# Optimization experiments

Hardware: AMD Instinct MI355X
Metric: run time of the kernel (lower is better)

## Reference

```python
import jax, jax.numpy as jnp
import numpy as np

BS, N, F, R, OUT = 8, 512, 512, 16, 512
ALPHA = 0.2

def setup_inputs() -> dict:
    key = jax.random.key(0)
    ks = jax.random.split(key, 16)
    w = lambda k, shp: (jax.random.normal(k, shp, dtype=jnp.float32) * 0.05)
    return {
        'x_ori': jax.random.normal(ks[0], (BS, N, F), dtype=jnp.float32),
        'x': jax.random.normal(ks[1], (BS, N, F), dtype=jnp.float32),
        'c': jax.random.normal(ks[2], (BS, 1, F), dtype=jnp.float32),
        'adj': jax.random.randint(ks[3], (BS, N, N, R), 0, 2, dtype=jnp.int32),
        'Wfc': w(ks[4], (F, F)),
        'Wdc': w(ks[5], (F, F)),
        'Wqv': w(ks[6], (2 * F, F)),
        'Wkv': w(ks[7], (2 * F, F)),
        'Wqc': w(ks[8], (F, F)),
        'Wkc': w(ks[9], (F, F)),
        'Wa': w(ks[10], (2 * F, R)),
        'Wu': w(ks[11], (2 * F, OUT)),
    }

def reference(x_ori, x, c, adj, Wfc, Wdc, Wqv, Wkv, Wqc, Wkc, Wa, Wu):
    # relation-context modulation vector m: [bs,1,F]
    m = jnp.matmul(jax.nn.elu(jnp.matmul(c, Wfc)), Wdc)
    nodes = jnp.concatenate([x, x_ori], axis=2)          # [bs,N,2F]
    xq = jnp.matmul(nodes, Wqv) * jnp.matmul(m, Wqc)     # [bs,N,F]
    xk = jnp.matmul(nodes, Wkv) * jnp.matmul(m, Wkc)     # [bs,N,F]
    # scores[b,i,j,r] = leakyrelu(xq_i . Wa[:F,r] + xk_j . Wa[F:,r])
    # (equivalent to cat([xq_i,xk_j]) @ Wa without materializing [bs,N,N,2F])
    sq = jnp.matmul(xq, Wa[:F])                          # [bs,N,R]
    sk = jnp.matmul(xk, Wa[F:])                          # [bs,N,R]
    scores = jax.nn.leaky_relu(sq[:, :, None, :] + sk[:, None, :, :], ALPHA)
    adj_f = adj.astype(scores.dtype)                     # [bs,N,N,R]
    s = jnp.sum(scores * adj_f, axis=3)                  # [bs,N,N]
    mask = jnp.sum(adj_f, axis=3) > 0
    attn = jax.nn.softmax(jnp.where(mask, s, jnp.float32(-9e15)), axis=2)
    new_x = jnp.matmul(attn, x)                          # [bs,N,F]
    return jnp.matmul(jnp.concatenate([x, new_x], axis=2), Wu)
```

## Files before the change

kernel.cpp:

```cpp
#include <hip/hip_runtime.h>
#include <hip/hip_bf16.h>
#include <cstddef>
#include <cstdint>

static constexpr int BSZ  = 8;
static constexpr int NN   = 512;
static constexpr int FF   = 512;
static constexpr int RR   = 16;
static constexpr int TWOF = 1024;

typedef __attribute__((ext_vector_type(8))) short short8;
typedef __attribute__((ext_vector_type(4))) float f32x4;

__device__ __forceinline__ ushort bf16_bits(float v) {
    union { __hip_bfloat16 h; ushort u; } cvt;
    cvt.h = __float2bfloat16(v);
    return cvt.u;
}

static constexpr size_t OFF_TB     = 0;
static constexpr size_t OFF_MB     = 16384;
static constexpr size_t OFF_MQ     = 32768;
static constexpr size_t OFF_MK     = 49152;
static constexpr size_t OFF_SQ     = 65536;
static constexpr size_t OFF_SK     = 327680;
static constexpr size_t OFF_WQET   = 589824;
static constexpr size_t OFF_WKET   = 851968;
static constexpr size_t OFF_ATTN   = 1114112;
static constexpr size_t OFF_XBF    = 5308416;
static constexpr size_t OFF_XTBF   = 9502720;
static constexpr size_t OFF_XORIBF = 13697024;
static constexpr size_t OFF_NEWXBF = 17891328;
static constexpr size_t OFF_WUT    = 22085632;

__global__ __launch_bounds__(256) void k_prep(
    const float* __restrict__ x_ori, const float* __restrict__ x,
    const float* __restrict__ Wu,
    ushort* __restrict__ xori_bf, ushort* __restrict__ x_bf,
    ushort* __restrict__ xT_bf, ushort* __restrict__ WuT)
{
    int blk = blockIdx.x;
    int t = threadIdx.x;
    if (blk < 1024) {
        int idx = blk * 256 + t;
        float4 a = ((const float4*)x_ori)[idx * 2];
        float4 b = ((const float4*)x_ori)[idx * 2 + 1];
        uint4 s;
        s.x = (uint)bf16_bits(a.x) | ((uint)bf16_bits(a.y) << 16);
        s.y = (uint)bf16_bits(a.z) | ((uint)bf16_bits(a.w) << 16);
        s.z = (uint)bf16_bits(b.x) | ((uint)bf16_bits(b.y) << 16);
        s.w = (uint)bf16_bits(b.z) | ((uint)bf16_bits(b.w) << 16);
        ((uint4*)xori_bf)[idx] = s;
    } else if (blk < 3072) {
        __shared__ float tile[32][33];
        int bb = blk - 1024;
        int f0 = (bb & 15) * 32, i0 = ((bb >> 4) & 15) * 32, b = bb >> 8;
        int cc = t & 31, r0 = t >> 5;
#pragma unroll
        for (int rr = 0; rr < 32; rr += 8) {
            int i = i0 + r0 + rr;
            float v = x[((size_t)b * NN + i) * FF + f0 + cc];
            tile[r0 + rr][cc] = v;
            x_bf[((size_t)b * NN + i) * FF + f0 + cc] = bf16_bits(v);
        }
        __syncthreads();
#pragma unroll
        for (int rr = 0; rr < 32; rr += 8) {
            int f = f0 + r0 + rr;
            xT_bf[((size_t)b * FF + f) * NN + i0 + cc] = bf16_bits(tile[cc][r0 + rr]);
        }
    } else {
        __shared__ float tile2[32][33];
        int bb = blk - 3072;
        int f0 = (bb & 31) * 32, o0 = (bb >> 5) * 32;
        int cc = t & 31, r0 = t >> 5;
#pragma unroll
        for (int rr = 0; rr < 32; rr += 8)
            tile2[r0 + rr][cc] = Wu[(size_t)(f0 + r0 + rr) * FF + o0 + cc];
        __syncthreads();
#pragma unroll
        for (int rr = 0; rr < 32; rr += 8)
            WuT[(size_t)(o0 + r0 + rr) * TWOF + f0 + cc] = bf16_bits(tile2[cc][r0 + rr]);
    }
}

__global__ __launch_bounds__(256) void k_matvec(const float* __restrict__ vin,
                                                const float* __restrict__ W,
                                                float* __restrict__ vout,
                                                int elu_out) {
    __shared__ float red[8][32];
    int b = blockIdx.y;
    int f0 = blockIdx.x * 32;
    int t = threadIdx.x;
    int f = t & 31, kq = t >> 5;
    const float* vb = vin + (size_t)b * FF;
    float acc = 0.f;
    int ks = kq * 64;
#pragma unroll 8
    for (int k = ks; k < ks + 64; ++k)
        acc = fmaf(vb[k], W[(size_t)k * FF + f0 + f], acc);
    red[kq][f] = acc;
    __syncthreads();
    if (kq == 0) {
        acc += red[1][f] + red[2][f] + red[3][f] + red[4][f] +
               red[5][f] + red[6][f] + red[7][f];
        if (elu_out) acc = (acc > 0.f) ? acc : expm1f(acc);
        vout[(size_t)b * FF + f0 + f] = acc;
    }
}

__global__ __launch_bounds__(256) void k_mqk(const float* __restrict__ m,
                                             const float* __restrict__ Wqc,
                                             const float* __restrict__ Wkc,
                                             float* __restrict__ mq,
                                             float* __restrict__ mk) {
    __shared__ float redq[8][32];
    __shared__ float redk[8][32];
    int b = blockIdx.y;
    int f0 = blockIdx.x * 32;
    int t = threadIdx.x;
    int f = t & 31, kq = t >> 5;
    const float* mb = m + (size_t)b * FF;
    float aq = 0.f, ak = 0.f;
    int ks = kq * 64;
#pragma unroll 8
    for (int k = ks; k < ks + 64; ++k) {
        float mv = mb[k];
        aq = fmaf(mv, Wqc[(size_t)k * FF + f0 + f], aq);
        ak = fmaf(mv, Wkc[(size_t)k * FF + f0 + f], ak);
    }
    redq[kq][f] = aq;
    redk[kq][f] = ak;
    __syncthreads();
    if (kq == 0) {
        aq += redq[1][f] + redq[2][f] + redq[3][f] + redq[4][f] +
              redq[5][f] + redq[6][f] + redq[7][f];
        ak += redk[1][f] + redk[2][f] + redk[3][f] + redk[4][f] +
              redk[5][f] + redk[6][f] + redk[7][f];
        mq[(size_t)b * FF + f0 + f] = aq;
        mk[(size_t)b * FF + f0 + f] = ak;
    }
}

__global__ __launch_bounds__(256) void k_weff(const float* __restrict__ Wqv,
                                              const float* __restrict__ Wkv,
                                              const float* __restrict__ Wa,
                                              const float* __restrict__ mqv,
                                              const float* __restrict__ mkv,
                                              ushort* __restrict__ WqEt,
                                              ushort* __restrict__ WkEt) {
    int z = blockIdx.z;
    const float* W = z ? Wkv : Wqv;
    const float* mvec = z ? mkv : mqv;
    ushort* WeffT = z ? WkEt : WqEt;
    int waRowOff = z ? FF : 0;

    __shared__ float4 wa4[FF * 4];
    int tid = threadIdx.x;
    int b = blockIdx.y;
    const float* mv = mvec + (size_t)b * FF;
#pragma unroll
    for (int qq = 0; qq < 8; ++qq) {
        int idx = tid + qq * 256;
        int f = idx >> 2, rq = idx & 3;
        float4 w = *reinterpret_cast<const float4*>(Wa + (size_t)(waRowOff + f) * RR + rq * 4);
        float s = mv[f];
        float4 o;
        o.x = w.x * s; o.y = w.y * s; o.z = w.z * s; o.w = w.w * s;
        wa4[idx] = o;
    }
    __syncthreads();
    int k_l = tid >> 2, r4 = tid & 3;
    int k = blockIdx.x * 64 + k_l;
    const float4* Wrow4 = reinterpret_cast<const float4*>(W + (size_t)k * FF);
    float4 acc = {0.f, 0.f, 0.f, 0.f};
#pragma unroll 4
    for (int f4 = 0; f4 < FF / 4; ++f4) {
        float4 w = Wrow4[f4];
        float4 v0 = wa4[(f4 * 4 + 0) * 4 + r4];
        float4 v1 = wa4[(f4 * 4 + 1) * 4 + r4];
        float4 v2 = wa4[(f4 * 4 + 2) * 4 + r4];
        float4 v3 = wa4[(f4 * 4 + 3) * 4 + r4];
        acc.x = fmaf(w.x, v0.x, acc.x); acc.y = fmaf(w.x, v0.y, acc.y);
        acc.z = fmaf(w.x, v0.z, acc.z); acc.w = fmaf(w.x, v0.w, acc.w);
        acc.x = fmaf(w.y, v1.x, acc.x); acc.y = fmaf(w.y, v1.y, acc.y);
        acc.z = fmaf(w.y, v1.z, acc.z); acc.w = fmaf(w.y, v1.w, acc.w);
        acc.x = fmaf(w.z, v2.x, acc.x); acc.y = fmaf(w.z, v2.y, acc.y);
        acc.z = fmaf(w.z, v2.z, acc.z); acc.w = fmaf(w.z, v2.w, acc.w);
        acc.x = fmaf(w.w, v3.x, acc.x); acc.y = fmaf(w.w, v3.y, acc.y);
        acc.z = fmaf(w.w, v3.z, acc.z); acc.w = fmaf(w.w, v3.w, acc.w);
    }
    WeffT[((size_t)b * RR + r4 * 4 + 0) * TWOF + k] = bf16_bits(acc.x);
    WeffT[((size_t)b * RR + r4 * 4 + 1) * TWOF + k] = bf16_bits(acc.y);
    WeffT[((size_t)b * RR + r4 * 4 + 2) * TWOF + k] = bf16_bits(acc.z);
    WeffT[((size_t)b * RR + r4 * 4 + 3) * TWOF + k] = bf16_bits(acc.w);
}

__global__ __launch_bounds__(256) void k_sqsk(const ushort* __restrict__ x_bf,
                                              const ushort* __restrict__ xori_bf,
                                              const ushort* __restrict__ WqEt,
                                              const ushort* __restrict__ WkEt,
                                              float* __restrict__ sq,
                                              float* __restrict__ sk) {
    int t = threadIdx.x;
    int b = blockIdx.y;
    int m0 = blockIdx.x * 32;
    int lane = t & 63, w = t >> 6;
    int sub = w & 1, isK = w >> 1;
    int m_l = lane & 15, q = lane >> 4;
    int row = m0 + sub * 16 + m_l;
    const ushort* Bt = (isK ? WkEt : WqEt) + ((size_t)b * RR + m_l) * TWOF;
    f32x4 acc = {0.f, 0.f, 0.f, 0.f};
#pragma unroll
    for (int k0 = 0; k0 < TWOF; k0 += 32) {
        const ushort* src = (k0 < FF) ? x_bf : xori_bf;
        int kc = k0 & (FF - 1);
        short8 af = *(const short8*)(src + ((size_t)b * NN + row) * FF + kc + q * 8);
        short8 bf = *(const short8*)(Bt + k0 + q * 8);
        acc = __builtin_amdgcn_mfma_f32_16x16x32_bf16(af, bf, acc, 0, 0, 0);
    }
    float* dst = isK ? sk : sq;
#pragma unroll
    for (int r = 0; r < 4; ++r) {
        int i = m0 + sub * 16 + q * 4 + r;
        dst[((size_t)b * NN + i) * RR + m_l] = acc[r];
    }
}

__global__ __launch_bounds__(256) void k_attn(const int* __restrict__ adj,
                                              const float* __restrict__ sq,
                                              const float* __restrict__ sk,
                                              ushort* __restrict__ attn_bf) {
    int t = threadIdx.x;
    int i = blockIdx.x;
    int b = blockIdx.y;
    __shared__ float sqv_s[RR];
    __shared__ float redmax[4];
    __shared__ float redsum[4];
    __shared__ float bc_max;
    __shared__ float bc_sum;
    if (t < RR) sqv_s[t] = sq[((size_t)b * NN + i) * RR + t];
    __syncthreads();
    float sv[RR];
#pragma unroll
    for (int r = 0; r < RR; ++r) sv[r] = sqv_s[r];

    float z[2];
#pragma unroll
    for (int jj = 0; jj < 2; ++jj) {
        int j = t + jj * 256;
        size_t base = ((size_t)(b * NN + i) * NN + j) * RR;
        const int4* ap = reinterpret_cast<const int4*>(adj + base);
        int4 a0 = ap[0], a1 = ap[1], a2 = ap[2], a3 = ap[3];
        const float4* kp = reinterpret_cast<const float4*>(sk + ((size_t)b * NN + j) * RR);
        float4 s0 = kp[0], s1 = kp[1], s2 = kp[2], s3 = kp[3];
        int sum_adj = a0.x + a0.y + a0.z + a0.w + a1.x + a1.y + a1.z + a1.w +
                      a2.x + a2.y + a2.z + a2.w + a3.x + a3.y + a3.z + a3.w;
        float ssum = 0.f;
#define LR_TERM(SVAL, AVAL, RIDX)                                   \
        { float v_ = sv[RIDX] + (SVAL);                             \
          v_ = fmaxf(v_, 0.2f * v_);                                \
          ssum = fmaf(v_, (float)(AVAL), ssum); }
        LR_TERM(s0.x, a0.x, 0)  LR_TERM(s0.y, a0.y, 1)
        LR_TERM(s0.z, a0.z, 2)  LR_TERM(s0.w, a0.w, 3)
        LR_TERM(s1.x, a1.x, 4)  LR_TERM(s1.y, a1.y, 5)
        LR_TERM(s1.z, a1.z, 6)  LR_TERM(s1.w, a1.w, 7)
        LR_TERM(s2.x, a2.x, 8)  LR_TERM(s2.y, a2.y, 9)
        LR_TERM(s2.z, a2.z, 10) LR_TERM(s2.w, a2.w, 11)
        LR_TERM(s3.x, a3.x, 12) LR_TERM(s3.y, a3.y, 13)
        LR_TERM(s3.z, a3.z, 14) LR_TERM(s3.w, a3.w, 15)
#undef LR_TERM
        z[jj] = (sum_adj > 0) ? ssum : -9e15f;
    }

    int wv = t >> 6, ln = t & 63;
    float lm = fmaxf(z[0], z[1]);
    for (int off = 32; off; off >>= 1) lm = fmaxf(lm, __shfl_xor(lm, off, 64));
    if (ln == 0) redmax[wv] = lm;
    __syncthreads();
    if (t == 0) bc_max = fmaxf(fmaxf(redmax[0], redmax[1]), fmaxf(redmax[2], redmax[3]));
    __syncthreads();
    float mx = bc_max;
    float e0 = __expf(z[0] - mx);
    float e1 = __expf(z[1] - mx);
    float ls = e0 + e1;
    for (int off = 32; off; off >>= 1) ls += __shfl_xor(ls, off, 64);
    if (ln == 0) redsum[wv] = ls;
    __syncthreads();
    if (t == 0) bc_sum = redsum[0] + redsum[1] + redsum[2] + redsum[3];
    __syncthreads();
    float inv = 1.f / bc_sum;
    ushort* outp = attn_bf + (size_t)(b * NN + i) * NN;
    outp[t] = bf16_bits(e0 * inv);
    outp[t + 256] = bf16_bits(e1 * inv);
}

__global__ __launch_bounds__(256) void k_gemm(const ushort* __restrict__ A1, size_t sA1,
                                              const ushort* __restrict__ A2, size_t sA2,
                                              const ushort* __restrict__ BT, size_t sBT,
                                              float* __restrict__ Cf,
                                              ushort* __restrict__ Cb, size_t sC,
                                              int K, int ldBT) {
    __shared__ ushort As[2][64 * 40];
    __shared__ ushort Bs[2][64 * 40];
    int t = threadIdx.x;
    int n0 = blockIdx.x * 64, m0 = blockIdx.y * 64, b = blockIdx.z;
    int row = t >> 2, c8 = (t & 3) * 8;
    int lane = t & 63, w = t >> 6;
    int m_l = lane & 15, q = lane >> 4;
    f32x4 acc[4] = {{0.f,0.f,0.f,0.f},{0.f,0.f,0.f,0.f},{0.f,0.f,0.f,0.f},{0.f,0.f,0.f,0.f}};
    const ushort* BTb = BT + (size_t)b * sBT;
    for (int k0 = 0; k0 < K; k0 += 64) {
#pragma unroll
        for (int h = 0; h < 2; ++h) {
            int kk = k0 + h * 32;
            const ushort* Aab; int kc;
            if (kk < FF) { Aab = A1 + (size_t)b * sA1; kc = kk; }
            else         { Aab = A2 + (size_t)b * sA2; kc = kk - FF; }
            uint4 av = *(const uint4*)(Aab + (size_t)(m0 + row) * FF + kc + c8);
            uint4 bv = *(const uint4*)(BTb + (size_t)(n0 + row) * ldBT + kk + c8);
            *(uint4*)(&As[h][row * 40 + c8]) = av;
            *(uint4*)(&Bs[h][row * 40 + c8]) = bv;
        }
        __syncthreads();
#pragma unroll
        for (int h = 0; h < 2; ++h) {
            short8 af = *(const short8*)(&As[h][(w * 16 + m_l) * 40 + q * 8]);
#pragma unroll
            for (int nb = 0; nb < 4; ++nb) {
                short8 bfr = *(const short8*)(&Bs[h][(nb * 16 + m_l) * 40 + q * 8]);
                acc[nb] = __builtin_amdgcn_mfma_f32_16x16x32_bf16(af, bfr, acc[nb], 0, 0, 0);
            }
        }
        __syncthreads();
    }
#pragma unroll
    for (int nb = 0; nb < 4; ++nb) {
#pragma unroll
        for (int r = 0; r < 4; ++r) {
            int mi = m0 + w * 16 + q * 4 + r;
            int ni = n0 + nb * 16 + m_l;
            float v = acc[nb][r];
            if (Cb) Cb[(size_t)b * sC + (size_t)mi * FF + ni] = bf16_bits(v);
            else    Cf[(size_t)b * sC + (size_t)mi * FF + ni] = v;
        }
    }
}

extern "C" void kernel_launch(void* const* d_in, const int* in_sizes, int n_in,
                              void* d_out, int out_size, void* d_ws, size_t ws_size,
                              hipStream_t stream) {
    const float* x_ori = (const float*)d_in[0];
    const float* x     = (const float*)d_in[1];
    const float* c     = (const float*)d_in[2];
    const int*   adj   = (const int*)d_in[3];
    const float* Wfc   = (const float*)d_in[4];
    const float* Wdc   = (const float*)d_in[5];
    const float* Wqv   = (const float*)d_in[6];
    const float* Wkv   = (const float*)d_in[7];
    const float* Wqc   = (const float*)d_in[8];
    const float* Wkc   = (const float*)d_in[9];
    const float* Wa    = (const float*)d_in[10];
    const float* Wu    = (const float*)d_in[11];
    float* out = (float*)d_out;

    char* ws = (char*)d_ws;
    float*  tb      = (float*)(ws + OFF_TB);
    float*  mb      = (float*)(ws + OFF_MB);
    float*  mq      = (float*)(ws + OFF_MQ);
    float*  mk      = (float*)(ws + OFF_MK);
    float*  sq      = (float*)(ws + OFF_SQ);
    float*  sk      = (float*)(ws + OFF_SK);
    ushort* WqEt    = (ushort*)(ws + OFF_WQET);
    ushort* WkEt    = (ushort*)(ws + OFF_WKET);
    ushort* attn_bf = (ushort*)(ws + OFF_ATTN);
    ushort* x_bf    = (ushort*)(ws + OFF_XBF);
    ushort* xT_bf   = (ushort*)(ws + OFF_XTBF);
    ushort* xori_bf = (ushort*)(ws + OFF_XORIBF);
    ushort* newx_bf = (ushort*)(ws + OFF_NEWXBF);
    ushort* WuT     = (ushort*)(ws + OFF_WUT);

    dim3 blk(256);

    k_prep<<<dim3(3584), blk, 0, stream>>>(x_ori, x, Wu, xori_bf, x_bf, xT_bf, WuT);

    k_matvec<<<dim3(16, BSZ), blk, 0, stream>>>(c, Wfc, tb, 1);
    k_matvec<<<dim3(16, BSZ), blk, 0, stream>>>(tb, Wdc, mb, 0);
    k_mqk<<<dim3(16, BSZ), blk, 0, stream>>>(mb, Wqc, Wkc, mq, mk);

    k_weff<<<dim3(16, BSZ, 2), blk, 0, stream>>>(Wqv, Wkv, Wa, mq, mk, WqEt, WkEt);

    k_sqsk<<<dim3(16, BSZ), blk, 0, stream>>>(x_bf, xori_bf, WqEt, WkEt, sq, sk);

    k_attn<<<dim3(NN, BSZ), blk, 0, stream>>>(adj, sq, sk, attn_bf);

    k_gemm<<<dim3(8, 8, BSZ), blk, 0, stream>>>(
        attn_bf, (size_t)NN * NN, attn_bf, (size_t)NN * NN,
        xT_bf, (size_t)FF * NN, nullptr, newx_bf, (size_t)NN * FF, FF, NN);

    k_gemm<<<dim3(8, 8, BSZ), blk, 0, stream>>>(
        x_bf, (size_t)NN * FF, newx_bf, (size_t)NN * FF,
        WuT, (size_t)0, out, nullptr, (size_t)NN * FF, TWOF, TWOF);
}
```

Baseline: 308.2 us.

## Fuse masked softmax with attention-times-x GEMM and fold first matvec into prep

Replaces the per-row softmax kernel and the separate attn@x GEMM with one kernel. Each block computes masked scores for 16 query rows, keeps the softmax numerators in LDS as bf16, and multiplies them by x^T with MFMA, applying the 1/rowsum scale at the end. This removes the materialized bf16 attention matrix, its global round trip and one launch. The first c@Wfc+ELU matvec also moves into the prep kernel as extra blocks, dropping another launch. In exchange the grid shrinks from 4096 blocks to 256, which lowers parallelism for streaming the large adj tensor. The PV stage also reads x^T straight from global memory with no LDS tiling.

```diff
diff --git a/kernel.cpp b/kernel.cpp
--- a/kernel.cpp
+++ b/kernel.cpp
@@ -26,7 +26,6 @@
 static constexpr size_t OFF_SK     = 327680;
 static constexpr size_t OFF_WQET   = 589824;
 static constexpr size_t OFF_WKET   = 851968;
-static constexpr size_t OFF_ATTN   = 1114112;
 static constexpr size_t OFF_XBF    = 5308416;
 static constexpr size_t OFF_XTBF   = 9502720;
 static constexpr size_t OFF_XORIBF = 13697024;
@@ -35,9 +34,11 @@
 
 __global__ __launch_bounds__(256) void k_prep(
     const float* __restrict__ x_ori, const float* __restrict__ x,
+    const float* __restrict__ c, const float* __restrict__ Wfc,
     const float* __restrict__ Wu,
     ushort* __restrict__ xori_bf, ushort* __restrict__ x_bf,
-    ushort* __restrict__ xT_bf, ushort* __restrict__ WuT)
+    ushort* __restrict__ xT_bf, ushort* __restrict__ WuT,
+    float* __restrict__ tb)
 {
     int blk = blockIdx.x;
     int t = threadIdx.x;
@@ -69,7 +70,7 @@
             int f = f0 + r0 + rr;
             xT_bf[((size_t)b * FF + f) * NN + i0 + cc] = bf16_bits(tile[cc][r0 + rr]);
         }
-    } else {
+    } else if (blk < 3584) {
         __shared__ float tile2[32][33];
         int bb = blk - 3072;
         int f0 = (bb & 31) * 32, o0 = (bb >> 5) * 32;
@@ -81,13 +82,30 @@
 #pragma unroll
         for (int rr = 0; rr < 32; rr += 8)
             WuT[(size_t)(o0 + r0 + rr) * TWOF + f0 + cc] = bf16_bits(tile2[cc][r0 + rr]);
+    } else {
+        __shared__ float red1[8][32];
+        int bb = blk - 3584;
+        int b = bb >> 4, f0 = (bb & 15) * 32;
+        int f = t & 31, kq = t >> 5;
+        const float* vb = c + (size_t)b * FF;
+        float acc = 0.f;
+        int ks = kq * 64;
+#pragma unroll 8
+        for (int k = ks; k < ks + 64; ++k)
+            acc = fmaf(vb[k], Wfc[(size_t)k * FF + f0 + f], acc);
+        red1[kq][f] = acc;
+        __syncthreads();
+        if (kq == 0) {
+            acc += red1[1][f] + red1[2][f] + red1[3][f] + red1[4][f] +
+                   red1[5][f] + red1[6][f] + red1[7][f];
+            tb[(size_t)b * FF + f0 + f] = (acc > 0.f) ? acc : expm1f(acc);
+        }
     }
 }
 
 __global__ __launch_bounds__(256) void k_matvec(const float* __restrict__ vin,
                                                 const float* __restrict__ W,
-                                                float* __restrict__ vout,
-                                                int elu_out) {
+                                                float* __restrict__ vout) {
     __shared__ float red[8][32];
     int b = blockIdx.y;
     int f0 = blockIdx.x * 32;
@@ -104,7 +122,6 @@
     if (kq == 0) {
         acc += red[1][f] + red[2][f] + red[3][f] + red[4][f] +
                red[5][f] + red[6][f] + red[7][f];
-        if (elu_out) acc = (acc > 0.f) ? acc : expm1f(acc);
         vout[(size_t)b * FF + f0 + f] = acc;
     }
 }
@@ -227,79 +244,113 @@
     }
 }
 
-__global__ __launch_bounds__(256) void k_attn(const int* __restrict__ adj,
-                                              const float* __restrict__ sq,
-                                              const float* __restrict__ sk,
-                                              ushort* __restrict__ attn_bf) {
-    int t = threadIdx.x;
-    int i = blockIdx.x;
+__global__ __launch_bounds__(256) void k_attn_pv(const int* __restrict__ adj,
+                                                 const float* __restrict__ sq,
+                                                 const float* __restrict__ sk,
+                                                 const ushort* __restrict__ xT_bf,
+                                                 ushort* __restrict__ newx_bf) {
+    constexpr int ZS = 520;
+    __shared__ float  zbuf[16 * ZS];
+    __shared__ ushort P[16 * ZS];
+    __shared__ float  rowsum[16];
+    int t = threadIdx.x;
     int b = blockIdx.y;
-    __shared__ float sqv_s[RR];
-    __shared__ float redmax[4];
-    __shared__ float redsum[4];
-    __shared__ float bc_max;
-    __shared__ float bc_sum;
-    if (t < RR) sqv_s[t] = sq[((size_t)b * NN + i) * RR + t];
+    int m0 = blockIdx.x * 16;
+
+    {
+        int r = t >> 4, cc = t & 15;
+        int i = m0 + r;
+        const float4* sqp = (const float4*)(sq + ((size_t)b * NN + i) * RR);
+        float4 q0 = sqp[0], q1 = sqp[1], q2 = sqp[2], q3 = sqp[3];
+        float sv[16] = {q0.x, q0.y, q0.z, q0.w, q1.x, q1.y, q1.z, q1.w,
+                        q2.x, q2.y, q2.z, q2.w, q3.x, q3.y, q3.z, q3.w};
+#pragma unroll 4
+        for (int it = 0; it < 32; ++it) {
+            int j = it * 16 + cc;
+            size_t base = (((size_t)b * NN + i) * NN + j) * RR;
+            const int4* ap = (const int4*)(adj + base);
+            int4 a0 = ap[0], a1 = ap[1], a2 = ap[2], a3 = ap[3];
+            const float4* kp = (const float4*)(sk + ((size_t)b * NN + j) * RR);
+            float4 s0 = kp[0], s1 = kp[1], s2 = kp[2], s3 = kp[3];
+            int sum_adj = a0.x + a0.y + a0.z + a0.w + a1.x + a1.y + a1.z + a1.w +
+                          a2.x + a2.y + a2.z + a2.w + a3.x + a3.y + a3.z + a3.w;
+            float ssum = 0.f;
+#define LR_TERM(SVAL, AVAL, RIDX)                                   \
+            { float v_ = sv[RIDX] + (SVAL);                         \
+              v_ = fmaxf(v_, 0.2f * v_);                            \
+              ssum = fmaf(v_, (float)(AVAL), ssum); }
+            LR_TERM(s0.x, a0.x, 0)  LR_TERM(s0.y, a0.y, 1)
+            LR_TERM(s0.z, a0.z, 2)  LR_TERM(s0.w, a0.w, 3)
+            LR_TERM(s1.x, a1.x, 4)  LR_TERM(s1.y, a1.y, 5)
+            LR_TERM(s1.z, a1.z, 6)  LR_TERM(s1.w, a1.w, 7)
+            LR_TERM(s2.x, a2.x, 8)  LR_TERM(s2.y, a2.y, 9)
+            LR_TERM(s2.z, a2.z, 10) LR_TERM(s2.w, a2.w, 11)
+            LR_TERM(s3.x, a3.x, 12) LR_TERM(s3.y, a3.y, 13)
+            LR_TERM(s3.z, a3.z, 14) LR_TERM(s3.w, a3.w, 15)
+#undef LR_TERM
+            zbuf[r * ZS + j] = (sum_adj > 0) ? ssum : -9e15f;
+        }
+    }
     __syncthreads();
-    float sv[RR];
-#pragma unroll
-    for (int r = 0; r < RR; ++r) sv[r] = sqv_s[r];
-
-    float z[2];
-#pragma unroll
-    for (int jj = 0; jj < 2; ++jj) {
-        int j = t + jj * 256;
-        size_t base = ((size_t)(b * NN + i) * NN + j) * RR;
-        const int4* ap = reinterpret_cast<const int4*>(adj + base);
-        int4 a0 = ap[0], a1 = ap[1], a2 = ap[2], a3 = ap[3];
-        const float4* kp = reinterpret_cast<const float4*>(sk + ((size_t)b * NN + j) * RR);
-        float4 s0 = kp[0], s1 = kp[1], s2 = kp[2], s3 = kp[3];
-        int sum_adj = a0.x + a0.y + a0.z + a0.w + a1.x + a1.y + a1.z + a1.w +
-                      a2.x + a2.y + a2.z + a2.w + a3.x + a3.y + a3.z + a3.w;
-        float ssum = 0.f;
-#define LR_TERM(SVAL, AVAL, RIDX)                                   \
-        { float v_ = sv[RIDX] + (SVAL);                             \
-          v_ = fmaxf(v_, 0.2f * v_);                                \
-          ssum = fmaf(v_, (float)(AVAL), ssum); }
-        LR_TERM(s0.x, a0.x, 0)  LR_TERM(s0.y, a0.y, 1)
-        LR_TERM(s0.z, a0.z, 2)  LR_TERM(s0.w, a0.w, 3)
-        LR_TERM(s1.x, a1.x, 4)  LR_TERM(s1.y, a1.y, 5)
-        LR_TERM(s1.z, a1.z, 6)  LR_TERM(s1.w, a1.w, 7)
-        LR_TERM(s2.x, a2.x, 8)  LR_TERM(s2.y, a2.y, 9)
-        LR_TERM(s2.z, a2.z, 10) LR_TERM(s2.w, a2.w, 11)
-        LR_TERM(s3.x, a3.x, 12) LR_TERM(s3.y, a3.y, 13)
-        LR_TERM(s3.z, a3.z, 14) LR_TERM(s3.w, a3.w, 15)
-#undef LR_TERM
-        z[jj] = (sum_adj > 0) ? ssum : -9e15f;
-    }
-
-    int wv = t >> 6, ln = t & 63;
-    float lm = fmaxf(z[0], z[1]);
-    for (int off = 32; off; off >>= 1) lm = fmaxf(lm, __shfl_xor(lm, off, 64));
-    if (ln == 0) redmax[wv] = lm;
+
+    {
+        int w = t >> 6, lane = t & 63;
+        int rr = w * 4 + (lane >> 4);
+        int cc = lane & 15;
+        const float* zr = &zbuf[rr * ZS];
+        float mx = -3.0e38f;
+#pragma unroll 8
+        for (int it = 0; it < 32; ++it) mx = fmaxf(mx, zr[it * 16 + cc]);
+#pragma unroll
+        for (int off = 1; off < 16; off <<= 1) mx = fmaxf(mx, __shfl_xor(mx, off, 64));
+        float sum = 0.f;
+        ushort* pr = &P[rr * ZS];
+#pragma unroll 8
+        for (int it = 0; it < 32; ++it) {
+            float e = __expf(zr[it * 16 + cc] - mx);
+            pr[it * 16 + cc] = bf16_bits(e);
+            sum += e;
+        }
+#pragma unroll
+        for (int off = 1; off < 16; off <<= 1) sum += __shfl_xor(sum, off, 64);
+        if (cc == 0) rowsum[rr] = sum;
+    }
     __syncthreads();
-    if (t == 0) bc_max = fmaxf(fmaxf(redmax[0], redmax[1]), fmaxf(redmax[2], redmax[3]));
-    __syncthreads();
-    float mx = bc_max;
-    float e0 = __expf(z[0] - mx);
-    float e1 = __expf(z[1] - mx);
-    float ls = e0 + e1;
-    for (int off = 32; off; off >>= 1) ls += __shfl_xor(ls, off, 64);
-    if (ln == 0) redsum[wv] = ls;
-    __syncthreads();
-    if (t == 0) bc_sum = redsum[0] + redsum[1] + redsum[2] + redsum[3];
-    __syncthreads();
-    float inv = 1.f / bc_sum;
-    ushort* outp = attn_bf + (size_t)(b * NN + i) * NN;
-    outp[t] = bf16_bits(e0 * inv);
-    outp[t + 256] = bf16_bits(e1 * inv);
+
+    {
+        int w = t >> 6, lane = t & 63;
+        int m_l = lane & 15, q = lane >> 4;
+        int n0w = w * 128;
+        f32x4 acc[8] = {};
+        const ushort* xTb = xT_bf + (size_t)b * FF * NN;
+        for (int k0 = 0; k0 < NN; k0 += 32) {
+            short8 af = *(const short8*)(&P[m_l * ZS + k0 + q * 8]);
+#pragma unroll
+            for (int nb = 0; nb < 8; ++nb) {
+                int n = n0w + nb * 16 + m_l;
+                short8 bfr = *(const short8*)(xTb + (size_t)n * NN + k0 + q * 8);
+                acc[nb] = __builtin_amdgcn_mfma_f32_16x16x32_bf16(af, bfr, acc[nb], 0, 0, 0);
+            }
+        }
+        float inv[4];
+#pragma unroll
+        for (int rg = 0; rg < 4; ++rg) inv[rg] = 1.f / rowsum[q * 4 + rg];
+#pragma unroll
+        for (int nb = 0; nb < 8; ++nb) {
+#pragma unroll
+            for (int rg = 0; rg < 4; ++rg) {
+                int i = m0 + q * 4 + rg;
+                int f = n0w + nb * 16 + m_l;
+                newx_bf[((size_t)b * NN + i) * FF + f] = bf16_bits(acc[nb][rg] * inv[rg]);
+            }
+        }
+    }
 }
 
 __global__ __launch_bounds__(256) void k_gemm(const ushort* __restrict__ A1, size_t sA1,
                                               const ushort* __restrict__ A2, size_t sA2,
                                               const ushort* __restrict__ BT, size_t sBT,
-                                              float* __restrict__ Cf,
-                                              ushort* __restrict__ Cb, size_t sC,
+                                              float* __restrict__ Cf, size_t sC,
                                               int K, int ldBT) {
     __shared__ ushort As[2][64 * 40];
     __shared__ ushort Bs[2][64 * 40];
@@ -340,9 +391,7 @@
         for (int r = 0; r < 4; ++r) {
             int mi = m0 + w * 16 + q * 4 + r;
             int ni = n0 + nb * 16 + m_l;
-            float v = acc[nb][r];
-            if (Cb) Cb[(size_t)b * sC + (size_t)mi * FF + ni] = bf16_bits(v);
-            else    Cf[(size_t)b * sC + (size_t)mi * FF + ni] = v;
+            Cf[(size_t)b * sC + (size_t)mi * FF + ni] = acc[nb][r];
         }
     }
 }
@@ -373,7 +422,6 @@
     float*  sk      = (float*)(ws + OFF_SK);
     ushort* WqEt    = (ushort*)(ws + OFF_WQET);
     ushort* WkEt    = (ushort*)(ws + OFF_WKET);
-    ushort* attn_bf = (ushort*)(ws + OFF_ATTN);
     ushort* x_bf    = (ushort*)(ws + OFF_XBF);
     ushort* xT_bf   = (ushort*)(ws + OFF_XTBF);
     ushort* xori_bf = (ushort*)(ws + OFF_XORIBF);
@@ -382,23 +430,19 @@
 
     dim3 blk(256);
 
-    k_prep<<<dim3(3584), blk, 0, stream>>>(x_ori, x, Wu, xori_bf, x_bf, xT_bf, WuT);
-
-    k_matvec<<<dim3(16, BSZ), blk, 0, stream>>>(c, Wfc, tb, 1);
-    k_matvec<<<dim3(16, BSZ), blk, 0, stream>>>(tb, Wdc, mb, 0);
+    k_prep<<<dim3(3712), blk, 0, stream>>>(x_ori, x, c, Wfc, Wu,
+                                           xori_bf, x_bf, xT_bf, WuT, tb);
+
+    k_matvec<<<dim3(16, BSZ), blk, 0, stream>>>(tb, Wdc, mb);
     k_mqk<<<dim3(16, BSZ), blk, 0, stream>>>(mb, Wqc, Wkc, mq, mk);
 
     k_weff<<<dim3(16, BSZ, 2), blk, 0, stream>>>(Wqv, Wkv, Wa, mq, mk, WqEt, WkEt);
 
     k_sqsk<<<dim3(16, BSZ), blk, 0, stream>>>(x_bf, xori_bf, WqEt, WkEt, sq, sk);
 
-    k_attn<<<dim3(NN, BSZ), blk, 0, stream>>>(adj, sq, sk, attn_bf);
-
-    k_gemm<<<dim3(8, 8, BSZ), blk, 0, stream>>>(
-        attn_bf, (size_t)NN * NN, attn_bf, (size_t)NN * NN,
-        xT_bf, (size_t)FF * NN, nullptr, newx_bf, (size_t)NN * FF, FF, NN);
+    k_attn_pv<<<dim3(32, BSZ), blk, 0, stream>>>(adj, sq, sk, xT_bf, newx_bf);
 
     k_gemm<<<dim3(8, 8, BSZ), blk, 0, stream>>>(
         x_bf, (size_t)NN * FF, newx_bf, (size_t)NN * FF,
-        WuT, (size_t)0, out, nullptr, (size_t)NN * FF, TWOF, TWOF);
-}
+        WuT, (size_t)0, out, (size_t)NN * FF, TWOF, TWOF);
+}
```

Result: no change. 302.9 us (-1.7%).
